# Optimization experiments

Measured on AMD Instinct MI355X. Metric: run time of the kernel, lower is better.

The kernel has to match this reference:

```python
import jax, jax.numpy as jnp
import numpy as np

IN_DIM = 128
HIDDEN = 128


def setup_inputs() -> dict:
    key = jax.random.key(0)
    k1, k2, k3, k4, k5 = jax.random.split(key, 5)
    bound_ih = 1.0 / np.sqrt(IN_DIM)
    bound_hh = 1.0 / np.sqrt(HIDDEN)
    return {
        "x": jax.random.normal(k1, (256, 2048, IN_DIM), dtype=jnp.float32),
        "W_ih": jax.random.uniform(k2, (HIDDEN, IN_DIM), minval=-bound_ih, maxval=bound_ih, dtype=jnp.float32),
        "b_ih": jax.random.uniform(k3, (HIDDEN,), minval=-bound_ih, maxval=bound_ih, dtype=jnp.float32),
        "W_hh": jax.random.uniform(k4, (HIDDEN, HIDDEN), minval=-bound_hh, maxval=bound_hh, dtype=jnp.float32),
        "b_hh": jax.random.uniform(k5, (HIDDEN,), minval=-bound_hh, maxval=bound_hh, dtype=jnp.float32),
    }


def reference(x, W_ih, b_ih, W_hh, b_hh):
    B, S, _ = x.shape
    # Precompute input projection for all timesteps in one big GEMM: [B,S,H]
    xw = jnp.einsum("bsi,hi->bsh", x, W_ih) + b_ih
    h0 = jnp.zeros((B, W_hh.shape[0]), dtype=x.dtype)

    def step(h, xw_t):
        h_new = jnp.tanh(xw_t + h @ W_hh.T + b_hh)
        return h_new, None

    # scan over time axis: move S to leading dim
    h_final, _ = jax.lax.scan(step, h0, jnp.swapaxes(xw, 0, 1))
    return h_final
```

## Files before the change

kernel.cpp:

```cpp
#include <hip/hip_runtime.h>


#define BATCH 256
#define SEQ   2048
#define HID   128
#define CH    16
#define NCHUNK (SEQ / CH)

template <int CTRL>
__device__ __forceinline__ float dpp_movf(float x) {
    return __int_as_float(__builtin_amdgcn_mov_dpp(__float_as_int(x), CTRL, 0xF, 0xF, true));
}

__device__ __forceinline__ float tanh_fast(float x) {
    x = fminf(fmaxf(x, -12.0f), 12.0f);
    float e = __expf(2.0f * x);
    return 1.0f - __fdividef(2.0f, e + 1.0f);
}

__global__ __launch_bounds__(512, 2) void rnn_scan_kernel(
    const float* __restrict__ x,
    const float* __restrict__ Wih,
    const float* __restrict__ bih,
    const float* __restrict__ Whh,
    const float* __restrict__ bhh,
    float* __restrict__ out)
{
    const int b = blockIdx.x;
    const int t = threadIdx.x;
    const int g = t >> 4;
    const int c = t & 15;
    const int colbase = c << 3;
    const int rowbase = g << 2;

    __shared__ __align__(16) float xbuf[2][CH * HID];
    __shared__ __align__(16) float hbuf[2][192];

    float4 wi[4][2], wh[4][2];
#pragma unroll
    for (int r = 0; r < 4; ++r) {
        const float* pi = Wih + (rowbase + r) * HID + colbase;
        const float* ph = Whh + (rowbase + r) * HID + colbase;
        wi[r][0] = *(const float4*)(pi);
        wi[r][1] = *(const float4*)(pi + 4);
        wh[r][0] = *(const float4*)(ph);
        wh[r][1] = *(const float4*)(ph + 4);
    }

    const int m = c & 3;
    const int o = ((m & 1) << 1) | ((m >> 1) & 1);
    const int row0 = rowbase + o;
    const float bias = bih[row0] + bhh[row0];
    const int hw = row0 + ((row0 >> 3) << 2);

    const int bx = (c >> 2) & 1;
    const int xoff0 = (((c << 1) ^ bx) << 2);
    const int xoff1 = ((((c << 1) | 1) ^ bx) << 2);
    const int sidx = t ^ ((t >> 3) & 1);

    const float* xsrc = x + (size_t)b * (SEQ * HID);

    {
        const float4* gp = (const float4*)xsrc;
        ((float4*)&xbuf[0][0])[sidx] = gp[t];
    }
    if (t < 192) hbuf[0][t] = 0.0f;
    __syncthreads();

    int cur = 0;
    for (int chn = 0; chn < NCHUNK; ++chn) {
        float4 q0;
        const bool pf = (chn + 1 < NCHUNK);
        if (pf) {
            const float4* gp = (const float4*)(xsrc + (size_t)(chn + 1) * (CH * HID));
            q0 = gp[t];
        }
        const float* xb = &xbuf[chn & 1][0];
#pragma unroll 1
        for (int s = 0; s < CH; ++s) {
            const float* xr = xb + s * HID;
            const float* hr = &hbuf[cur][12 * c];
            float4 hv0 = *(const float4*)(hr);
            float4 hv1 = *(const float4*)(hr + 4);
            float4 xv0 = *(const float4*)(xr + xoff0);
            float4 xv1 = *(const float4*)(xr + xoff1);

            float a[4];
#pragma unroll
            for (int r = 0; r < 4; ++r) {
                float acc;
                acc = wi[r][0].x * xv0.x;
                acc = fmaf(wi[r][0].y, xv0.y, acc);
                acc = fmaf(wi[r][0].z, xv0.z, acc);
                acc = fmaf(wi[r][0].w, xv0.w, acc);
                acc = fmaf(wi[r][1].x, xv1.x, acc);
                acc = fmaf(wi[r][1].y, xv1.y, acc);
                acc = fmaf(wi[r][1].z, xv1.z, acc);
                acc = fmaf(wi[r][1].w, xv1.w, acc);
                acc = fmaf(wh[r][0].x, hv0.x, acc);
                acc = fmaf(wh[r][0].y, hv0.y, acc);
                acc = fmaf(wh[r][0].z, hv0.z, acc);
                acc = fmaf(wh[r][0].w, hv0.w, acc);
                acc = fmaf(wh[r][1].x, hv1.x, acc);
                acc = fmaf(wh[r][1].y, hv1.y, acc);
                acc = fmaf(wh[r][1].z, hv1.z, acc);
                acc = fmaf(wh[r][1].w, hv1.w, acc);
                a[r] = acc;
            }

            const bool b0 = (c & 1) != 0;
            const bool b1 = (c & 2) != 0;
            float k0 = b0 ? a[2] : a[0], s0 = b0 ? a[0] : a[2];
            float k1 = b0 ? a[3] : a[1], s1 = b0 ? a[1] : a[3];
            float t0 = k0 + dpp_movf<0xB1>(s0);
            float t1 = k1 + dpp_movf<0xB1>(s1);
            float k2 = b1 ? t1 : t0, s2 = b1 ? t0 : t1;
            float u = k2 + dpp_movf<0x4E>(s2);
            u += dpp_movf<0x124>(u);
            u += dpp_movf<0x128>(u);

            float h = tanh_fast(u + bias);
            if (c < 4) {
                hbuf[cur ^ 1][hw] = h;
            }

            if (s == CH - 1 && pf) {
                ((float4*)&xbuf[(chn + 1) & 1][0])[sidx] = q0;
            }
            __syncthreads();
            cur ^= 1;
        }
    }
    if (t < HID) out[(size_t)b * HID + t] = hbuf[cur][t + ((t >> 3) << 2)];
}

extern "C" void kernel_launch(void* const* d_in, const int* in_sizes, int n_in,
                              void* d_out, int out_size, void* d_ws, size_t ws_size,
                              hipStream_t stream) {
    const float* x   = (const float*)d_in[0];
    const float* Wih = (const float*)d_in[1];
    const float* bih = (const float*)d_in[2];
    const float* Whh = (const float*)d_in[3];
    const float* bhh = (const float*)d_in[4];
    float* out = (float*)d_out;

    rnn_scan_kernel<<<BATCH, 512, 0, stream>>>(x, Wih, bih, Whh, bhh, out);
}
```

Measured before the change: 1.106 ms.

## Batch 16 sequences per block and use split-bf16 MFMA for recurrence

Replaces the per-sequence scalar FMA/DPP recurrence with a block handling 16 batch rows, computing both input and hidden projections with bf16 MFMA 16x16x32 using a hi/lo split (three MFMAs) to approximate fp32 accuracy. The input projection for the next chunk is computed while the current chunk's recurrence runs, and x is prefetched two chunks ahead into swizzled LDS. Only 16 blocks are launched, so most CUs sit idle, and per-step latency is now set by the MFMA chain plus a barrier. The hi/lo split also carries some precision risk.

```diff
diff --git a/kernel.cpp b/kernel.cpp
--- a/kernel.cpp
+++ b/kernel.cpp
@@ -4,18 +4,26 @@
 #define BATCH 256
 #define SEQ   2048
 #define HID   128
-#define CH    16
+#define CH    8
 #define NCHUNK (SEQ / CH)
-
-template <int CTRL>
-__device__ __forceinline__ float dpp_movf(float x) {
-    return __int_as_float(__builtin_amdgcn_mov_dpp(__float_as_int(x), CTRL, 0xF, 0xF, true));
-}
+#define BPB   16
+
+typedef __attribute__((ext_vector_type(8))) short bf16x8;
+typedef __attribute__((ext_vector_type(4))) float f32x4;
 
 __device__ __forceinline__ float tanh_fast(float x) {
     x = fminf(fmaxf(x, -12.0f), 12.0f);
     float e = __expf(2.0f * x);
     return 1.0f - __fdividef(2.0f, e + 1.0f);
+}
+
+__device__ __forceinline__ void bf16_split(float v, short& hi, short& lo) {
+    unsigned u = __float_as_uint(v);
+    unsigned hb = (u + 0x8000u) & 0xFFFF0000u;
+    float hf = __uint_as_float(hb);
+    float r = v - hf;
+    hi = (short)(hb >> 16);
+    lo = (short)((__float_as_uint(r) + 0x8000u) >> 16);
 }
 
 __global__ __launch_bounds__(512, 2) void rnn_scan_kernel(
@@ -26,112 +34,181 @@
     const float* __restrict__ bhh,
     float* __restrict__ out)
 {
-    const int b = blockIdx.x;
+    const int b0 = blockIdx.x * BPB;
     const int t = threadIdx.x;
-    const int g = t >> 4;
-    const int c = t & 15;
-    const int colbase = c << 3;
-    const int rowbase = g << 2;
-
-    __shared__ __align__(16) float xbuf[2][CH * HID];
-    __shared__ __align__(16) float hbuf[2][192];
-
-    float4 wi[4][2], wh[4][2];
+    const int lane = t & 63;
+    const int w = t >> 6;
+    const int l15 = lane & 15;
+    const int l16 = lane >> 4;
+
+    __shared__ __align__(16) ushort xlds[2][2][CH][BPB][HID];
+    __shared__ __align__(16) ushort hlds[2][2][BPB][HID];
+    char* const xbase = (char*)&xlds[0][0][0][0][0];
+    char* const hbase = (char*)&hlds[0][0][0][0];
+
+    const int nc = (w << 4) + l15;
+    const float biasv = bih[nc] + bhh[nc];
+    const f32x4 bias4 = {biasv, biasv, biasv, biasv};
+    bf16x8 wih_h[4], wih_l[4], whh_h[4], whh_l[4];
+    auto build_frag = [&](const float* src, bf16x8& fh, bf16x8& fl) {
+        float4 u0 = *(const float4*)(src);
+        float4 u1 = *(const float4*)(src + 4);
+        short hh, ll;
+        bf16_split(u0.x, hh, ll); fh[0] = hh; fl[0] = ll;
+        bf16_split(u0.y, hh, ll); fh[1] = hh; fl[1] = ll;
+        bf16_split(u0.z, hh, ll); fh[2] = hh; fl[2] = ll;
+        bf16_split(u0.w, hh, ll); fh[3] = hh; fl[3] = ll;
+        bf16_split(u1.x, hh, ll); fh[4] = hh; fl[4] = ll;
+        bf16_split(u1.y, hh, ll); fh[5] = hh; fl[5] = ll;
+        bf16_split(u1.z, hh, ll); fh[6] = hh; fl[6] = ll;
+        bf16_split(u1.w, hh, ll); fh[7] = hh; fl[7] = ll;
+    };
+#pragma unroll
+    for (int kk = 0; kk < 4; ++kk) {
+        build_frag(Wih + nc * HID + kk * 32 + (l16 << 3), wih_h[kk], wih_l[kk]);
+        build_frag(Whh + nc * HID + kk * 32 + (l16 << 3), whh_h[kk], whh_l[kk]);
+    }
+
+    const int swzA = (l15 & 7) << 4;
+    char* px[2][4];
+    char* ph[4];
+#pragma unroll
+    for (int kk = 0; kk < 4; ++kk) {
+        const int av = l15 * 256 + (((kk * 64) + (l16 * 16)) ^ swzA);
+        px[0][kk] = xbase + av;
+        px[1][kk] = xbase + 65536 + av;
+        ph[kk]    = hbase + av;
+    }
+    char* whp[4];
 #pragma unroll
     for (int r = 0; r < 4; ++r) {
-        const float* pi = Wih + (rowbase + r) * HID + colbase;
-        const float* ph = Whh + (rowbase + r) * HID + colbase;
-        wi[r][0] = *(const float4*)(pi);
-        wi[r][1] = *(const float4*)(pi + 4);
-        wh[r][0] = *(const float4*)(ph);
-        wh[r][1] = *(const float4*)(ph + 4);
-    }
-
-    const int m = c & 3;
-    const int o = ((m & 1) << 1) | ((m >> 1) & 1);
-    const int row0 = rowbase + o;
-    const float bias = bih[row0] + bhh[row0];
-    const int hw = row0 + ((row0 >> 3) << 2);
-
-    const int bx = (c >> 2) & 1;
-    const int xoff0 = (((c << 1) ^ bx) << 2);
-    const int xoff1 = ((((c << 1) | 1) ^ bx) << 2);
-    const int sidx = t ^ ((t >> 3) & 1);
-
-    const float* xsrc = x + (size_t)b * (SEQ * HID);
+        const int mr = (l16 << 2) + r;
+        whp[r] = hbase + ((mr * 256 + nc * 2) ^ ((mr & 7) << 4));
+    }
+    const int bt = t >> 5;
+    const int wsoff = bt * 256 + ((((t & 31) << 3)) ^ ((bt & 7) << 4));
+    char* ws[2] = { xbase + wsoff, xbase + 65536 + wsoff };
+
+    const float* xg = x + (size_t)(b0 + bt) * (SEQ * HID) + ((t & 31) << 2);
+
+    auto write_tile = [&](char* wp, int tile, float4 v) {
+        unsigned u0 = __float_as_uint(v.x), u1 = __float_as_uint(v.y);
+        unsigned u2 = __float_as_uint(v.z), u3 = __float_as_uint(v.w);
+        unsigned h0 = u0 & 0xFFFF0000u, h1 = u1 & 0xFFFF0000u;
+        unsigned h2 = u2 & 0xFFFF0000u, h3 = u3 & 0xFFFF0000u;
+        uint2 hp, lp;
+        hp.x = (u0 >> 16) | h1;
+        hp.y = (u2 >> 16) | h3;
+        float l0f = v.x - __uint_as_float(h0), l1f = v.y - __uint_as_float(h1);
+        float l2f = v.z - __uint_as_float(h2), l3f = v.w - __uint_as_float(h3);
+        lp.x = (__float_as_uint(l0f) >> 16) | (__float_as_uint(l1f) & 0xFFFF0000u);
+        lp.y = (__float_as_uint(l2f) >> 16) | (__float_as_uint(l3f) & 0xFFFF0000u);
+        *(uint2*)(wp + tile * 4096)         = hp;
+        *(uint2*)(wp + 32768 + tile * 4096) = lp;
+    };
+
+    float4 qc0, qc1;
+#pragma unroll
+    for (int cc = 0; cc < 2; ++cc) {
+        const float* pgc = xg + cc * (CH * HID);
+#pragma unroll
+        for (int s = 0; s < CH; ++s) {
+            float4 q = *(const float4*)(pgc + s * HID);
+            write_tile(ws[cc], s, q);
+            if (cc == 1 && s == 6) qc0 = q;
+            if (cc == 1 && s == 7) qc1 = q;
+        }
+    }
+    ((float4*)hbase)[t] = make_float4(0.f, 0.f, 0.f, 0.f);
+    __syncthreads();
+
+    f32x4 xwA[CH], xwB[CH];
+#pragma unroll
+    for (int s = 0; s < CH; ++s) {
+        f32x4 c0 = bias4, c1 = {0,0,0,0}, c2 = {0,0,0,0};
+#pragma unroll
+        for (int kk = 0; kk < 4; ++kk) {
+            bf16x8 xh = *(const bf16x8*)(px[0][kk] + s * 4096);
+            bf16x8 xl = *(const bf16x8*)(px[0][kk] + 32768 + s * 4096);
+            c0 = __builtin_amdgcn_mfma_f32_16x16x32_bf16(xh, wih_h[kk], c0, 0, 0, 0);
+            c1 = __builtin_amdgcn_mfma_f32_16x16x32_bf16(xh, wih_l[kk], c1, 0, 0, 0);
+            c2 = __builtin_amdgcn_mfma_f32_16x16x32_bf16(xl, wih_h[kk], c2, 0, 0, 0);
+        }
+        xwA[s] = c0 + c1 + c2;
+    }
+    const float* pgm = xg + 2 * (CH * HID);
+
+#define CHUNK_BODY(nn, PAR, xwc, xwn)                                          \
+    {                                                                          \
+        const bool gx = (nn) + 1 < NCHUNK;                                     \
+        const bool gs = (nn) + 2 < NCHUNK;                                     \
+        float4 q[CH];                                                          \
+        _Pragma("unroll")                                                      \
+        for (int s = 0; s < CH; ++s) {                                         \
+            if (gs) q[s] = *(const float4*)(pgm + s * HID);                    \
+            if (s == 0) { if (gx) write_tile(ws[(PAR) ^ 1], 6, qc0); }         \
+            if (s == 1) { if (gx) write_tile(ws[(PAR) ^ 1], 7, qc1); }         \
+            if (s >= 2) { if (gs) write_tile(ws[PAR], s - 2, q[s - 2]); }      \
+            {                 \
+                const int p = s & 1;                                           \
+                f32x4 a0 = xwc[s], a1 = {0,0,0,0}, a2 = {0,0,0,0};             \
+                _Pragma("unroll")                                              \
+                for (int kk = 0; kk < 4; ++kk) {                               \
+                    bf16x8 hh = *(const bf16x8*)(ph[kk] + p * 8192);           \
+                    bf16x8 hl = *(const bf16x8*)(ph[kk] + p * 8192 + 4096);    \
+                    a0 = __builtin_amdgcn_mfma_f32_16x16x32_bf16(hh, whh_h[kk], a0, 0, 0, 0); \
+                    a1 = __builtin_amdgcn_mfma_f32_16x16x32_bf16(hh, whh_l[kk], a1, 0, 0, 0); \
+                    a2 = __builtin_amdgcn_mfma_f32_16x16x32_bf16(hl, whh_h[kk], a2, 0, 0, 0); \
+                }                                                              \
+                f32x4 u4 = a0 + a1 + a2;                                       \
+                _Pragma("unroll")                                              \
+                for (int r = 0; r < 4; ++r) {                                  \
+                    float hv = tanh_fast(u4[r]);                               \
+                    unsigned ub = __float_as_uint(hv);                         \
+                    unsigned hb = ub & 0xFFFF0000u;                            \
+                    float lf = hv - __uint_as_float(hb);                       \
+                    *(ushort*)(whp[r] + ((p ^ 1) * 8192)) = (ushort)(ub >> 16); \
+                    *(ushort*)(whp[r] + ((p ^ 1) * 8192 + 4096)) =             \
+                        (ushort)(__float_as_uint(lf) >> 16);                   \
+                }                                                              \
+            }                                                                  \
+            if (gx) {         \
+                f32x4 c0 = bias4, c1 = {0,0,0,0}, c2 = {0,0,0,0};              \
+                _Pragma("unroll")                                              \
+                for (int kk = 0; kk < 4; ++kk) {                               \
+                    bf16x8 xh = *(const bf16x8*)(px[(PAR) ^ 1][kk] + s * 4096); \
+                    bf16x8 xl = *(const bf16x8*)(px[(PAR) ^ 1][kk] + 32768 + s * 4096); \
+                    c0 = __builtin_amdgcn_mfma_f32_16x16x32_bf16(xh, wih_h[kk], c0, 0, 0, 0); \
+                    c1 = __builtin_amdgcn_mfma_f32_16x16x32_bf16(xh, wih_l[kk], c1, 0, 0, 0); \
+                    c2 = __builtin_amdgcn_mfma_f32_16x16x32_bf16(xl, wih_h[kk], c2, 0, 0, 0); \
+                }                                                              \
+                xwn[s] = c0 + c1 + c2;                                         \
+            }                                                                  \
+            __syncthreads();                                                   \
+        }                                                                      \
+        if (gs) { qc0 = q[6]; qc1 = q[7]; }                                    \
+        pgm += CH * HID;                                                       \
+    }
+
+#pragma unroll 1
+    for (int nn = 0; nn < NCHUNK; nn += 2) {
+        CHUNK_BODY(nn,     0, xwA, xwB);
+        CHUNK_BODY(nn + 1, 1, xwB, xwA);
+    }
+#undef CHUNK_BODY
 
     {
-        const float4* gp = (const float4*)xsrc;
-        ((float4*)&xbuf[0][0])[sidx] = gp[t];
-    }
-    if (t < 192) hbuf[0][t] = 0.0f;
-    __syncthreads();
-
-    int cur = 0;
-    for (int chn = 0; chn < NCHUNK; ++chn) {
-        float4 q0;
-        const bool pf = (chn + 1 < NCHUNK);
-        if (pf) {
-            const float4* gp = (const float4*)(xsrc + (size_t)(chn + 1) * (CH * HID));
-            q0 = gp[t];
-        }
-        const float* xb = &xbuf[chn & 1][0];
-#pragma unroll 1
-        for (int s = 0; s < CH; ++s) {
-            const float* xr = xb + s * HID;
-            const float* hr = &hbuf[cur][12 * c];
-            float4 hv0 = *(const float4*)(hr);
-            float4 hv1 = *(const float4*)(hr + 4);
-            float4 xv0 = *(const float4*)(xr + xoff0);
-            float4 xv1 = *(const float4*)(xr + xoff1);
-
-            float a[4];
-#pragma unroll
-            for (int r = 0; r < 4; ++r) {
-                float acc;
-                acc = wi[r][0].x * xv0.x;
-                acc = fmaf(wi[r][0].y, xv0.y, acc);
-                acc = fmaf(wi[r][0].z, xv0.z, acc);
-                acc = fmaf(wi[r][0].w, xv0.w, acc);
-                acc = fmaf(wi[r][1].x, xv1.x, acc);
-                acc = fmaf(wi[r][1].y, xv1.y, acc);
-                acc = fmaf(wi[r][1].z, xv1.z, acc);
-                acc = fmaf(wi[r][1].w, xv1.w, acc);
-                acc = fmaf(wh[r][0].x, hv0.x, acc);
-                acc = fmaf(wh[r][0].y, hv0.y, acc);
-                acc = fmaf(wh[r][0].z, hv0.z, acc);
-                acc = fmaf(wh[r][0].w, hv0.w, acc);
-                acc = fmaf(wh[r][1].x, hv1.x, acc);
-                acc = fmaf(wh[r][1].y, hv1.y, acc);
-                acc = fmaf(wh[r][1].z, hv1.z, acc);
-                acc = fmaf(wh[r][1].w, hv1.w, acc);
-                a[r] = acc;
-            }
-
-            const bool b0 = (c & 1) != 0;
-            const bool b1 = (c & 2) != 0;
-            float k0 = b0 ? a[2] : a[0], s0 = b0 ? a[0] : a[2];
-            float k1 = b0 ? a[3] : a[1], s1 = b0 ? a[1] : a[3];
-            float t0 = k0 + dpp_movf<0xB1>(s0);
-            float t1 = k1 + dpp_movf<0xB1>(s1);
-            float k2 = b1 ? t1 : t0, s2 = b1 ? t0 : t1;
-            float u = k2 + dpp_movf<0x4E>(s2);
-            u += dpp_movf<0x124>(u);
-            u += dpp_movf<0x128>(u);
-
-            float h = tanh_fast(u + bias);
-            if (c < 4) {
-                hbuf[cur ^ 1][hw] = h;
-            }
-
-            if (s == CH - 1 && pf) {
-                ((float4*)&xbuf[(chn + 1) & 1][0])[sidx] = q0;
-            }
-            __syncthreads();
-            cur ^= 1;
-        }
-    }
-    if (t < HID) out[(size_t)b * HID + t] = hbuf[cur][t + ((t >> 3) << 2)];
+        const int c4 = (t & 31) << 2;
+        const int rd = bt * 256 + ((((t & 31) << 3)) ^ ((bt & 7) << 4));
+        uint2 hp = *(const uint2*)(hbase + rd);
+        uint2 lp = *(const uint2*)(hbase + rd + 4096);
+        float4 o;
+        o.x = __uint_as_float(hp.x << 16) + __uint_as_float(lp.x << 16);
+        o.y = __uint_as_float(hp.x & 0xFFFF0000u) + __uint_as_float(lp.x & 0xFFFF0000u);
+        o.z = __uint_as_float(hp.y << 16) + __uint_as_float(lp.y << 16);
+        o.w = __uint_as_float(hp.y & 0xFFFF0000u) + __uint_as_float(lp.y & 0xFFFF0000u);
+        *(float4*)(out + (size_t)(b0 + bt) * HID + c4) = o;
+    }
 }
 
 extern "C" void kernel_launch(void* const* d_in, const int* in_sizes, int n_in,
@@ -144,5 +221,5 @@
     const float* bhh = (const float*)d_in[4];
     float* out = (float*)d_out;
 
-    rnn_scan_kernel<<<BATCH, 512, 0, stream>>>(x, Wih, bih, Whh, bhh, out);
-}
+    rnn_scan_kernel<<<BATCH / BPB, 512, 0, stream>>>(x, Wih, bih, Whh, bhh, out);
+}
```

Result: slower. 3.825 ms (+245.9%).
